# Performance work log

Measured on AMD Instinct MI355X. Metric: run time of the kernel, lower is better.

## Reference

```python
import jax, jax.numpy as jnp
import numpy as np

E = 8          # num experts
D = 1024       # hidden/model dim
H = 4096
B, S = 4, 2048


def setup_inputs() -> dict:
    key = jax.random.key(0)
    ks = jax.random.split(key, 4)
    x = jax.random.normal(ks[0], (B, S, D), dtype=jnp.float32)
    Wg = jax.random.normal(ks[1], (D, E), dtype=jnp.float32) * (1.0 / np.sqrt(D))
    W1 = jax.random.normal(ks[2], (E, D, H), dtype=jnp.float32) * (1.0 / np.sqrt(D))
    b1 = jnp.zeros((E, H), dtype=jnp.float32)
    W2 = jax.random.normal(ks[3], (E, H, D), dtype=jnp.float32) * (1.0 / np.sqrt(H))
    b2 = jnp.zeros((E, D), dtype=jnp.float32)
    return {"x": x, "Wg": Wg, "W1": W1, "b1": b1, "W2": W2, "b2": b2, "top_k": 2}


def reference(x, Wg, W1, b1, W2, b2, top_k):
    b, s, d = x.shape
    xt = x.reshape(-1, d)  # [T, D], T = total tokens
    # Linear gating: softmax over expert logits, select top_k, renormalize
    logits = xt @ Wg                                   # [T, E]
    probs = jax.nn.softmax(logits, axis=-1)            # [T, E]
    vals, idx = jax.lax.top_k(probs, top_k)            # [T, k]
    vals = vals / jnp.sum(vals, axis=-1, keepdims=True)
    # Combine weights: zero except at selected experts
    combine = jnp.sum(jax.nn.one_hot(idx, E, dtype=probs.dtype) * vals[..., None], axis=1)  # [T, E]
    # FFN experts (MLP with gelu), computed densely across experts
    h = jax.nn.gelu(jnp.einsum('td,edh->eth', xt, W1) + b1[:, None, :])  # [E, T, H]
    y = jnp.einsum('eth,ehd->etd', h, W2) + b2[:, None, :]               # [E, T, D]
    out = jnp.einsum('te,etd->td', combine, y)                           # [T, D]
    return out.reshape(b, s, d)
```

## Files before the change

### kernel.cpp

```cpp
#include <hip/hip_runtime.h>

#define T_TOK 8192
#define DIM   1024
#define HDIM  4096
#define NE    8
#define BK    64
#define BM    128
#define BN    128
#define SLOT_CAP (T_TOK * 2 + NE * BM)
#define TILES (SLOT_CAP / BM)

typedef float        f32x4 __attribute__((ext_vector_type(4)));
typedef unsigned int u32x4 __attribute__((ext_vector_type(4)));

__device__ inline unsigned short f2bf(float f) {
  union { float f; unsigned int u; } a; a.f = f;
  unsigned int u = a.u;
  unsigned int r = (u + 0x7FFFu + ((u >> 16) & 1u)) >> 16;
  return (unsigned short)r;
}

__device__ inline f32x4 mfma_bf16_16x16x32(u32x4 a, u32x4 b, f32x4 c) {
  asm("v_mfma_f32_16x16x32_bf16 %0, %1, %2, %0" : "+v"(c) : "v"(a), "v"(b));
  return c;
}

__device__ inline void gload_lds16(const void* g, void* l) {
  __builtin_amdgcn_global_load_lds(
      (const __attribute__((address_space(1))) void*)g,
      (__attribute__((address_space(3))) void*)l, 16, 0, 0);
}

__device__ inline float gelu_fast(float v) {
  const float c2 = 1.5957691216057308f;
  float z = c2 * (v + 0.044715f * v * v * v);
  return v / (1.0f + __expf(-z));
}

__global__ __launch_bounds__(256) void transpose_bf16_kernel(const float* __restrict__ src,
                                                             unsigned short* __restrict__ dst,
                                                             int R, int C) {
  __shared__ float tile[64][65];
  int e  = blockIdx.z;
  int c0 = blockIdx.x * 64, r0 = blockIdx.y * 64;
  int c  = threadIdx.x & 63, r4 = threadIdx.x >> 6;
  const float* s = src + (size_t)e * R * C;
#pragma unroll
  for (int i = 0; i < 16; i++) {
    int r = r4 + i * 4;
    tile[r][c] = s[(size_t)(r0 + r) * C + (c0 + c)];
  }
  __syncthreads();
  int cc = (threadIdx.x & 31) * 2;
  int rb = threadIdx.x >> 5;
  unsigned short* d = dst + (size_t)e * R * C;
#pragma unroll
  for (int i = 0; i < 8; i++) {
    int rr = rb + i * 8;
    unsigned int p = (unsigned int)f2bf(tile[cc][rr])
                   | ((unsigned int)f2bf(tile[cc + 1][rr]) << 16);
    *(unsigned int*)(d + (size_t)(c0 + rr) * R + (r0 + cc)) = p;
  }
}

__global__ __launch_bounds__(256) void routing_kernel(const float* __restrict__ x,
                                                      const float* __restrict__ Wg,
                                                      int* __restrict__ tok_e,
                                                      float* __restrict__ tok_w,
                                                      unsigned short* __restrict__ xb) {
  int tok  = (blockIdx.x * 256 + threadIdx.x) >> 6;
  int lane = threadIdx.x & 63;
  const float* xr = x + (size_t)tok * DIM;
  float acc[NE];
#pragma unroll
  for (int e = 0; e < NE; e++) acc[e] = 0.f;
  for (int d = lane; d < DIM; d += 64) {
    float xv = xr[d];
    const float* wr = Wg + d * NE;
#pragma unroll
    for (int e = 0; e < NE; e++) acc[e] += xv * wr[e];
  }
#pragma unroll
  for (int e = 0; e < NE; e++) {
#pragma unroll
    for (int off = 32; off > 0; off >>= 1) acc[e] += __shfl_xor(acc[e], off);
  }
  if (lane == 0) {
    int i0 = 0;
#pragma unroll
    for (int e = 1; e < NE; e++) if (acc[e] > acc[i0]) i0 = e;
    int i1 = (i0 == 0) ? 1 : 0;
#pragma unroll
    for (int e = 0; e < NE; e++) if (e != i0 && acc[e] > acc[i1]) i1 = e;
    float w0 = 1.0f / (1.0f + expf(acc[i1] - acc[i0]));
    tok_e[tok * 2]     = i0;
    tok_e[tok * 2 + 1] = i1;
    tok_w[tok * 2]     = w0;
    tok_w[tok * 2 + 1] = 1.0f - w0;
  }
  unsigned short* xo = xb + (size_t)tok * DIM;
#pragma unroll
  for (int i = 0; i < 4; i++) {
    f32x4 v = *(const f32x4*)(xr + lane * 16 + i * 4);
    unsigned long long p = (unsigned long long)f2bf(v[0])
                         | ((unsigned long long)f2bf(v[1]) << 16)
                         | ((unsigned long long)f2bf(v[2]) << 32)
                         | ((unsigned long long)f2bf(v[3]) << 48);
    *(unsigned long long*)(xo + lane * 16 + i * 4) = p;
  }
}

__global__ __launch_bounds__(256) void count_kernel(const int* __restrict__ tok_e,
                                                    int* __restrict__ counts) {
  __shared__ int h[NE];
  if (threadIdx.x < NE) h[threadIdx.x] = 0;
  __syncthreads();
  for (int i = blockIdx.x * 256 + threadIdx.x; i < T_TOK * 2; i += 32 * 256)
    atomicAdd(&h[tok_e[i]], 1);
  __syncthreads();
  if (threadIdx.x < NE) atomicAdd(&counts[threadIdx.x], h[threadIdx.x]);
}

__global__ void offsets_kernel(const int* __restrict__ counts, int* __restrict__ offs) {
  if (threadIdx.x == 0 && blockIdx.x == 0) {
    int acc = 0; offs[0] = 0;
    for (int e = 0; e < NE; e++) {
      acc += (counts[e] + BM - 1) / BM * BM;
      offs[e + 1] = acc;
    }
  }
}

__global__ __launch_bounds__(256) void scatter_kernel(const int* __restrict__ tok_e,
                                                      const int* __restrict__ offs,
                                                      int* __restrict__ cursors,
                                                      int* __restrict__ slot_token,
                                                      int* __restrict__ tok_slot) {
  int t = blockIdx.x * 256 + threadIdx.x;
  int lane = threadIdx.x & 63;
#pragma unroll
  for (int j = 0; j < 2; j++) {
    int e = tok_e[t * 2 + j];
#pragma unroll
    for (int ee = 0; ee < NE; ee++) {
      unsigned long long m = __ballot(e == ee);
      if (e == ee) {
        int leader = __ffsll(m) - 1;
        int base = 0;
        if (lane == leader) base = atomicAdd(&cursors[ee], (int)__popcll(m));
        base = __shfl(base, leader);
        int pos = base + (int)__popcll(m & ((1ULL << lane) - 1ULL));
        int s = offs[ee] + pos;
        slot_token[s] = t;
        tok_slot[t * 2 + j] = s;
      }
    }
  }
}


__global__ __launch_bounds__(256) void gemm1_kernel(const unsigned short* __restrict__ Xb,
                                                    const unsigned short* __restrict__ W1T,
                                                    const float* __restrict__ b1,
                                                    const int* __restrict__ slot_token,
                                                    const int* __restrict__ offs,
                                                    unsigned short* __restrict__ Hbuf) {
  __shared__ __align__(16) unsigned short As[BM][BK];
  __shared__ __align__(16) unsigned short Bs[BN][BK];
  const int GY = HDIM / BN;
  int lin = blockIdx.y * gridDim.x + blockIdx.x;
  int cpx = (TILES * GY) >> 3;
  int wk  = (lin & 7) * cpx + (lin >> 3);
  int bx = wk / GY, by = wk % GY;

  int row0 = bx * BM;
  if (row0 >= offs[NE]) return;
  int e = 0;
#pragma unroll
  for (int i = 1; i < NE; i++) if (row0 >= offs[i]) e = i;
  int n0  = by * BN;
  int tid  = threadIdx.x;
  int lane = tid & 63;
  int w    = tid >> 6;
  int wr = tid >> 7;
  int wc = (tid >> 6) & 1;

  int lr  = lane >> 3;
  int lcx = (lane & 7) ^ lr;
  const unsigned short* aG[4];
  const unsigned short* bG[4];
  unsigned short* aL[4];
  unsigned short* bL[4];
#pragma unroll
  for (int i = 0; i < 4; i++) {
    int r = w * 32 + i * 8;
    int tk = slot_token[row0 + r + lr];
    if (tk < 0) tk = 0;
    aG[i] = Xb + (size_t)tk * DIM + lcx * 8;
    bG[i] = W1T + ((size_t)e * HDIM + n0 + r + lr) * DIM + lcx * 8;
    aL[i] = &As[r][0];
    bL[i] = &Bs[r][0];
  }

  int frow = lane & 15;
  int hi   = lane >> 4;
  int kxs  = (hi * 8) ^ ((lane & 7) << 3);

  f32x4 acc[4][4];
#pragma unroll
  for (int m = 0; m < 4; m++)
#pragma unroll
    for (int n = 0; n < 4; n++) acc[m][n] = 0.f;

  for (int k0 = 0; k0 < DIM; k0 += BK) {
#pragma unroll
    for (int i = 0; i < 4; i++) gload_lds16(aG[i] + k0, aL[i]);
#pragma unroll
    for (int i = 0; i < 4; i++) gload_lds16(bG[i] + k0, bL[i]);
    __syncthreads();
#pragma unroll
    for (int kk = 0; kk < 2; kk++) {
      int col = (kk * 32) ^ kxs;
      u32x4 a[4], b[4];
#pragma unroll
      for (int m = 0; m < 4; m++)
        a[m] = *(const u32x4*)&As[wr * 64 + m * 16 + frow][col];
#pragma unroll
      for (int n = 0; n < 4; n++)
        b[n] = *(const u32x4*)&Bs[wc * 64 + n * 16 + frow][col];
#pragma unroll
      for (int m = 0; m < 4; m++)
#pragma unroll
        for (int n = 0; n < 4; n++)
          acc[m][n] = mfma_bf16_16x16x32(a[m], b[n], acc[m][n]);
    }
    __syncthreads();
  }

  float bias[4];
#pragma unroll
  for (int n = 0; n < 4; n++) bias[n] = b1[e * HDIM + n0 + wc * 64 + n * 16 + frow];
  unsigned short (*E)[136] = (unsigned short (*)[136])(&As[0][0]);
#pragma unroll
  for (int c0 = 0; c0 < 128; c0 += 32) {
    if (wr == (c0 >> 6)) {
      int mbase = (c0 & 63) >> 4;
#pragma unroll
      for (int mm = 0; mm < 2; mm++) {
        int m = mbase + mm;
#pragma unroll
        for (int n = 0; n < 4; n++)
#pragma unroll
          for (int j = 0; j < 4; j++)
            E[mm * 16 + hi * 4 + j][wc * 64 + n * 16 + frow] =
                f2bf(gelu_fast(acc[m][n][j] + bias[n]));
      }
    }
    __syncthreads();
#pragma unroll
    for (int p = 0; p < 2; p++) {
      int r  = p * 16 + (tid >> 4);
      int cc = (tid & 15) * 8;
      u32x4 v = *(const u32x4*)&E[r][cc];
      *(u32x4*)(Hbuf + (size_t)(row0 + c0 + r) * HDIM + n0 + cc) = v;
    }
    __syncthreads();
  }
}

__global__ __launch_bounds__(256) void gemm2_kernel(const unsigned short* __restrict__ Hbuf,
                                                    const unsigned short* __restrict__ W2T,
                                                    const float* __restrict__ b2,
                                                    const int* __restrict__ offs,
                                                    float* __restrict__ Ybuf) {
  __shared__ __align__(16) unsigned short As[BM][BK];
  __shared__ __align__(16) unsigned short Bs[BN][BK];
  const int GY = DIM / BN;
  int lin = blockIdx.y * gridDim.x + blockIdx.x;
  int cpx = (TILES * GY) >> 3;
  int wk  = (lin & 7) * cpx + (lin >> 3);
  int bx = wk / GY, by = wk % GY;

  int row0 = bx * BM;
  if (row0 >= offs[NE]) return;
  int e = 0;
#pragma unroll
  for (int i = 1; i < NE; i++) if (row0 >= offs[i]) e = i;
  int n0  = by * BN;
  int tid  = threadIdx.x;
  int lane = tid & 63;
  int w    = tid >> 6;
  int wr = tid >> 7;
  int wc = (tid >> 6) & 1;

  int lr  = lane >> 3;
  int lcx = (lane & 7) ^ lr;
  const unsigned short* aG[4];
  const unsigned short* bG[4];
  unsigned short* aL[4];
  unsigned short* bL[4];
#pragma unroll
  for (int i = 0; i < 4; i++) {
    int r = w * 32 + i * 8;
    aG[i] = Hbuf + (size_t)(row0 + r + lr) * HDIM + lcx * 8;
    bG[i] = W2T + ((size_t)e * DIM + n0 + r + lr) * HDIM + lcx * 8;
    aL[i] = &As[r][0];
    bL[i] = &Bs[r][0];
  }

  int frow = lane & 15;
  int kxs  = ((lane >> 4) * 8) ^ ((lane & 7) << 3);

  f32x4 acc[4][4];
#pragma unroll
  for (int m = 0; m < 4; m++)
#pragma unroll
    for (int n = 0; n < 4; n++) acc[m][n] = 0.f;

  for (int k0 = 0; k0 < HDIM; k0 += BK) {
#pragma unroll
    for (int i = 0; i < 4; i++) gload_lds16(aG[i] + k0, aL[i]);
#pragma unroll
    for (int i = 0; i < 4; i++) gload_lds16(bG[i] + k0, bL[i]);
    __syncthreads();
#pragma unroll
    for (int kk = 0; kk < 2; kk++) {
      int col = (kk * 32) ^ kxs;
      u32x4 a[4], b[4];
#pragma unroll
      for (int m = 0; m < 4; m++)
        a[m] = *(const u32x4*)&As[wr * 64 + m * 16 + frow][col];
#pragma unroll
      for (int n = 0; n < 4; n++)
        b[n] = *(const u32x4*)&Bs[wc * 64 + n * 16 + frow][col];
#pragma unroll
      for (int m = 0; m < 4; m++)
#pragma unroll
        for (int n = 0; n < 4; n++)
          acc[m][n] = mfma_bf16_16x16x32(a[m], b[n], acc[m][n]);
    }
    __syncthreads();
  }

  int rbase = (lane >> 4) * 4;
  int cbase = lane & 15;
#pragma unroll
  for (int m = 0; m < 4; m++) {
#pragma unroll
    for (int n = 0; n < 4; n++) {
      int dcol = n0 + wc * 64 + n * 16 + cbase;
      float bias = b2[e * DIM + dcol];
#pragma unroll
      for (int j = 0; j < 4; j++) {
        int gr = row0 + wr * 64 + m * 16 + rbase + j;
        Ybuf[(size_t)gr * DIM + dcol] = acc[m][n][j] + bias;
      }
    }
  }
}

__global__ __launch_bounds__(256) void combine_kernel(const float* __restrict__ Ybuf,
                                                      const int* __restrict__ tok_slot,
                                                      const float* __restrict__ tok_w,
                                                      float* __restrict__ out) {
  int t = blockIdx.x;
  int c = threadIdx.x * 4;
  int s0 = tok_slot[t * 2], s1 = tok_slot[t * 2 + 1];
  float w0 = tok_w[t * 2], w1 = tok_w[t * 2 + 1];
  f32x4 y0 = *(const f32x4*)(Ybuf + (size_t)s0 * DIM + c);
  f32x4 y1 = *(const f32x4*)(Ybuf + (size_t)s1 * DIM + c);
  f32x4 r;
#pragma unroll
  for (int i = 0; i < 4; i++) r[i] = w0 * y0[i] + w1 * y1[i];
  *(f32x4*)(out + (size_t)t * DIM + c) = r;
}

extern "C" void kernel_launch(void* const* d_in, const int* in_sizes, int n_in,
                              void* d_out, int out_size, void* d_ws, size_t ws_size,
                              hipStream_t stream) {
  (void)in_sizes; (void)n_in; (void)out_size;
  const float* x  = (const float*)d_in[0];
  const float* Wg = (const float*)d_in[1];
  const float* W1 = (const float*)d_in[2];
  const float* b1 = (const float*)d_in[3];
  const float* W2 = (const float*)d_in[4];
  const float* b2 = (const float*)d_in[5];
  float* out = (float*)d_out;

  char* ws = (char*)d_ws;
  size_t off = 0;
  auto take = [&](size_t bytes) -> char* {
    char* p = ws + off;
    off += (bytes + 255) & ~(size_t)255;
    return p;
  };
  unsigned short* W1T  = (unsigned short*)take((size_t)NE * DIM * HDIM * 2);
  unsigned short* W2T  = (unsigned short*)take((size_t)NE * DIM * HDIM * 2);
  unsigned short* Xb   = (unsigned short*)take((size_t)T_TOK * DIM * 2);
  unsigned short* Hbuf = (unsigned short*)take((size_t)SLOT_CAP * HDIM * 2);
  float* Ybuf       = (float*)take((size_t)SLOT_CAP * DIM * 4);
  int*   slot_token = (int*)take(SLOT_CAP * 4);
  int*   tok_e      = (int*)take(T_TOK * 2 * 4);
  float* tok_w      = (float*)take(T_TOK * 2 * 4);
  int*   tok_slot   = (int*)take(T_TOK * 2 * 4);
  int*   counts     = (int*)take(256);
  int*   cursors    = (int*)take(256);
  int*   offs       = (int*)take(256);

  if (off > ws_size) {
    hipMemsetAsync(d_out, 0, (size_t)out_size * 4, stream);
    return;
  }

  hipMemsetAsync(counts, 0, 256, stream);
  hipMemsetAsync(cursors, 0, 256, stream);
  hipMemsetAsync(slot_token, 0xFF, SLOT_CAP * 4, stream);

  routing_kernel<<<T_TOK / 4, 256, 0, stream>>>(x, Wg, tok_e, tok_w, Xb);
  count_kernel<<<32, 256, 0, stream>>>(tok_e, counts);
  offsets_kernel<<<1, 64, 0, stream>>>(counts, offs);
  scatter_kernel<<<T_TOK / 256, 256, 0, stream>>>(tok_e, offs, cursors, slot_token, tok_slot);
  transpose_bf16_kernel<<<dim3(HDIM / 64, DIM / 64, NE), 256, 0, stream>>>(W1, W1T, DIM, HDIM);
  transpose_bf16_kernel<<<dim3(DIM / 64, HDIM / 64, NE), 256, 0, stream>>>(W2, W2T, HDIM, DIM);
  gemm1_kernel<<<dim3(TILES, HDIM / BN), 256, 0, stream>>>(Xb, W1T, b1, slot_token, offs, Hbuf);
  gemm2_kernel<<<dim3(TILES, DIM / BN), 256, 0, stream>>>(Hbuf, W2T, b2, offs, Ybuf);
  combine_kernel<<<T_TOK, 256, 0, stream>>>(Ybuf, tok_slot, tok_w, out);
}
```

Baseline: 534.8 us.

## Fuse expert counting into routing, store Y in bf16, vectorize transpose writes

Expert histogram counting moves into the routing kernel, and the offsets kernel is removed by having each consumer compute offsets from the counts. The gemm2 output is staged through LDS and stored as bf16 with 16-byte writes, which halves Ybuf traffic, and the combine kernel reads that bf16. The transpose kernel writes 16-byte vectors instead of 4-byte ones. Together these cut two kernel launches and memory traffic, at the cost of extra rounding of expert outputs to bf16 before the weighted combine.

```diff
diff --git a/kernel.cpp b/kernel.cpp
--- a/kernel.cpp
+++ b/kernel.cpp
@@ -37,6 +37,13 @@
   return v / (1.0f + __expf(-z));
 }
 
+__device__ inline void load_offs(const int* __restrict__ counts, int* offs) {
+  offs[0] = 0;
+#pragma unroll
+  for (int e = 0; e < NE; e++)
+    offs[e + 1] = offs[e] + ((counts[e] + BM - 1) / BM) * BM;
+}
+
 __global__ __launch_bounds__(256) void transpose_bf16_kernel(const float* __restrict__ src,
                                                              unsigned short* __restrict__ dst,
                                                              int R, int C) {
@@ -51,15 +58,17 @@
     tile[r][c] = s[(size_t)(r0 + r) * C + (c0 + c)];
   }
   __syncthreads();
-  int cc = (threadIdx.x & 31) * 2;
-  int rb = threadIdx.x >> 5;
   unsigned short* d = dst + (size_t)e * R * C;
-#pragma unroll
-  for (int i = 0; i < 8; i++) {
-    int rr = rb + i * 8;
-    unsigned int p = (unsigned int)f2bf(tile[cc][rr])
-                   | ((unsigned int)f2bf(tile[cc + 1][rr]) << 16);
-    *(unsigned int*)(d + (size_t)(c0 + rr) * R + (r0 + cc)) = p;
+  int rbase = (threadIdx.x & 7) * 8;
+#pragma unroll
+  for (int g = 0; g < 2; g++) {
+    int cc = (threadIdx.x >> 3) + g * 32;
+    u32x4 v;
+#pragma unroll
+    for (int k = 0; k < 4; k++)
+      v[k] = (unsigned int)f2bf(tile[rbase + 2 * k][cc])
+           | ((unsigned int)f2bf(tile[rbase + 2 * k + 1][cc]) << 16);
+    *(u32x4*)(d + (size_t)(c0 + cc) * R + (r0 + rbase)) = v;
   }
 }
 
@@ -67,7 +76,11 @@
                                                       const float* __restrict__ Wg,
                                                       int* __restrict__ tok_e,
                                                       float* __restrict__ tok_w,
-                                                      unsigned short* __restrict__ xb) {
+                                                      unsigned short* __restrict__ xb,
+                                                      int* __restrict__ counts) {
+  __shared__ int h[NE];
+  if (threadIdx.x < NE) h[threadIdx.x] = 0;
+  __syncthreads();
   int tok  = (blockIdx.x * 256 + threadIdx.x) >> 6;
   int lane = threadIdx.x & 63;
   const float* xr = x + (size_t)tok * DIM;
@@ -97,6 +110,8 @@
     tok_e[tok * 2 + 1] = i1;
     tok_w[tok * 2]     = w0;
     tok_w[tok * 2 + 1] = 1.0f - w0;
+    atomicAdd(&h[i0], 1);
+    atomicAdd(&h[i1], 1);
   }
   unsigned short* xo = xb + (size_t)tok * DIM;
 #pragma unroll
@@ -108,34 +123,17 @@
                          | ((unsigned long long)f2bf(v[3]) << 48);
     *(unsigned long long*)(xo + lane * 16 + i * 4) = p;
   }
-}
-
-__global__ __launch_bounds__(256) void count_kernel(const int* __restrict__ tok_e,
-                                                    int* __restrict__ counts) {
-  __shared__ int h[NE];
-  if (threadIdx.x < NE) h[threadIdx.x] = 0;
-  __syncthreads();
-  for (int i = blockIdx.x * 256 + threadIdx.x; i < T_TOK * 2; i += 32 * 256)
-    atomicAdd(&h[tok_e[i]], 1);
   __syncthreads();
   if (threadIdx.x < NE) atomicAdd(&counts[threadIdx.x], h[threadIdx.x]);
 }
 
-__global__ void offsets_kernel(const int* __restrict__ counts, int* __restrict__ offs) {
-  if (threadIdx.x == 0 && blockIdx.x == 0) {
-    int acc = 0; offs[0] = 0;
-    for (int e = 0; e < NE; e++) {
-      acc += (counts[e] + BM - 1) / BM * BM;
-      offs[e + 1] = acc;
-    }
-  }
-}
-
 __global__ __launch_bounds__(256) void scatter_kernel(const int* __restrict__ tok_e,
-                                                      const int* __restrict__ offs,
+                                                      const int* __restrict__ counts,
                                                       int* __restrict__ cursors,
                                                       int* __restrict__ slot_token,
                                                       int* __restrict__ tok_slot) {
+  int offs[NE + 1];
+  load_offs(counts, offs);
   int t = blockIdx.x * 256 + threadIdx.x;
   int lane = threadIdx.x & 63;
 #pragma unroll
@@ -163,10 +161,12 @@
                                                     const unsigned short* __restrict__ W1T,
                                                     const float* __restrict__ b1,
                                                     const int* __restrict__ slot_token,
-                                                    const int* __restrict__ offs,
+                                                    const int* __restrict__ counts,
                                                     unsigned short* __restrict__ Hbuf) {
   __shared__ __align__(16) unsigned short As[BM][BK];
   __shared__ __align__(16) unsigned short Bs[BN][BK];
+  int offs[NE + 1];
+  load_offs(counts, offs);
   const int GY = HDIM / BN;
   int lin = blockIdx.y * gridDim.x + blockIdx.x;
   int cpx = (TILES * GY) >> 3;
@@ -271,10 +271,12 @@
 __global__ __launch_bounds__(256) void gemm2_kernel(const unsigned short* __restrict__ Hbuf,
                                                     const unsigned short* __restrict__ W2T,
                                                     const float* __restrict__ b2,
-                                                    const int* __restrict__ offs,
-                                                    float* __restrict__ Ybuf) {
+                                                    const int* __restrict__ counts,
+                                                    unsigned short* __restrict__ Ybuf) {
   __shared__ __align__(16) unsigned short As[BM][BK];
   __shared__ __align__(16) unsigned short Bs[BN][BK];
+  int offs[NE + 1];
+  load_offs(counts, offs);
   const int GY = DIM / BN;
   int lin = blockIdx.y * gridDim.x + blockIdx.x;
   int cpx = (TILES * GY) >> 3;
@@ -309,7 +311,8 @@
   }
 
   int frow = lane & 15;
-  int kxs  = ((lane >> 4) * 8) ^ ((lane & 7) << 3);
+  int hi   = lane >> 4;
+  int kxs  = (hi * 8) ^ ((lane & 7) << 3);
 
   f32x4 acc[4][4];
 #pragma unroll
@@ -342,37 +345,59 @@
     __syncthreads();
   }
 
-  int rbase = (lane >> 4) * 4;
-  int cbase = lane & 15;
-#pragma unroll
-  for (int m = 0; m < 4; m++) {
-#pragma unroll
-    for (int n = 0; n < 4; n++) {
-      int dcol = n0 + wc * 64 + n * 16 + cbase;
-      float bias = b2[e * DIM + dcol];
-#pragma unroll
-      for (int j = 0; j < 4; j++) {
-        int gr = row0 + wr * 64 + m * 16 + rbase + j;
-        Ybuf[(size_t)gr * DIM + dcol] = acc[m][n][j] + bias;
+  float bias[4];
+#pragma unroll
+  for (int n = 0; n < 4; n++) bias[n] = b2[e * DIM + n0 + wc * 64 + n * 16 + frow];
+  unsigned short (*E)[136] = (unsigned short (*)[136])(&As[0][0]);
+#pragma unroll
+  for (int c0 = 0; c0 < 128; c0 += 32) {
+    if (wr == (c0 >> 6)) {
+      int mbase = (c0 & 63) >> 4;
+#pragma unroll
+      for (int mm = 0; mm < 2; mm++) {
+        int m = mbase + mm;
+#pragma unroll
+        for (int n = 0; n < 4; n++)
+#pragma unroll
+          for (int j = 0; j < 4; j++)
+            E[mm * 16 + hi * 4 + j][wc * 64 + n * 16 + frow] =
+                f2bf(acc[m][n][j] + bias[n]);
       }
     }
-  }
-}
-
-__global__ __launch_bounds__(256) void combine_kernel(const float* __restrict__ Ybuf,
+    __syncthreads();
+#pragma unroll
+    for (int p = 0; p < 2; p++) {
+      int r  = p * 16 + (tid >> 4);
+      int cc = (tid & 15) * 8;
+      u32x4 v = *(const u32x4*)&E[r][cc];
+      *(u32x4*)(Ybuf + (size_t)(row0 + c0 + r) * DIM + n0 + cc) = v;
+    }
+    __syncthreads();
+  }
+}
+
+__global__ __launch_bounds__(256) void combine_kernel(const unsigned short* __restrict__ Ybuf,
                                                       const int* __restrict__ tok_slot,
                                                       const float* __restrict__ tok_w,
                                                       float* __restrict__ out) {
-  int t = blockIdx.x;
-  int c = threadIdx.x * 4;
+  int t = blockIdx.x * 2 + (threadIdx.x >> 7);
+  int c = (threadIdx.x & 127) * 8;
   int s0 = tok_slot[t * 2], s1 = tok_slot[t * 2 + 1];
   float w0 = tok_w[t * 2], w1 = tok_w[t * 2 + 1];
-  f32x4 y0 = *(const f32x4*)(Ybuf + (size_t)s0 * DIM + c);
-  f32x4 y1 = *(const f32x4*)(Ybuf + (size_t)s1 * DIM + c);
-  f32x4 r;
-#pragma unroll
-  for (int i = 0; i < 4; i++) r[i] = w0 * y0[i] + w1 * y1[i];
-  *(f32x4*)(out + (size_t)t * DIM + c) = r;
+  u32x4 y0 = *(const u32x4*)(Ybuf + (size_t)s0 * DIM + c);
+  u32x4 y1 = *(const u32x4*)(Ybuf + (size_t)s1 * DIM + c);
+  float r[8];
+#pragma unroll
+  for (int k = 0; k < 4; k++) {
+    union { unsigned int u; float f; } a0, b0, a1, b1;
+    a0.u = y0[k] << 16; b0.u = y0[k] & 0xFFFF0000u;
+    a1.u = y1[k] << 16; b1.u = y1[k] & 0xFFFF0000u;
+    r[2 * k]     = w0 * a0.f + w1 * a1.f;
+    r[2 * k + 1] = w0 * b0.f + w1 * b1.f;
+  }
+  float* o = out + (size_t)t * DIM + c;
+  *(f32x4*)o       = *(f32x4*)&r[0];
+  *(f32x4*)(o + 4) = *(f32x4*)&r[4];
 }
 
 extern "C" void kernel_launch(void* const* d_in, const int* in_sizes, int n_in,
@@ -398,14 +423,13 @@
   unsigned short* W2T  = (unsigned short*)take((size_t)NE * DIM * HDIM * 2);
   unsigned short* Xb   = (unsigned short*)take((size_t)T_TOK * DIM * 2);
   unsigned short* Hbuf = (unsigned short*)take((size_t)SLOT_CAP * HDIM * 2);
-  float* Ybuf       = (float*)take((size_t)SLOT_CAP * DIM * 4);
+  unsigned short* Ybuf = (unsigned short*)take((size_t)SLOT_CAP * DIM * 2);
   int*   slot_token = (int*)take(SLOT_CAP * 4);
   int*   tok_e      = (int*)take(T_TOK * 2 * 4);
   float* tok_w      = (float*)take(T_TOK * 2 * 4);
   int*   tok_slot   = (int*)take(T_TOK * 2 * 4);
   int*   counts     = (int*)take(256);
   int*   cursors    = (int*)take(256);
-  int*   offs       = (int*)take(256);
 
   if (off > ws_size) {
     hipMemsetAsync(d_out, 0, (size_t)out_size * 4, stream);
@@ -416,13 +440,11 @@
   hipMemsetAsync(cursors, 0, 256, stream);
   hipMemsetAsync(slot_token, 0xFF, SLOT_CAP * 4, stream);
 
-  routing_kernel<<<T_TOK / 4, 256, 0, stream>>>(x, Wg, tok_e, tok_w, Xb);
-  count_kernel<<<32, 256, 0, stream>>>(tok_e, counts);
-  offsets_kernel<<<1, 64, 0, stream>>>(counts, offs);
-  scatter_kernel<<<T_TOK / 256, 256, 0, stream>>>(tok_e, offs, cursors, slot_token, tok_slot);
+  routing_kernel<<<T_TOK / 4, 256, 0, stream>>>(x, Wg, tok_e, tok_w, Xb, counts);
+  scatter_kernel<<<T_TOK / 256, 256, 0, stream>>>(tok_e, counts, cursors, slot_token, tok_slot);
   transpose_bf16_kernel<<<dim3(HDIM / 64, DIM / 64, NE), 256, 0, stream>>>(W1, W1T, DIM, HDIM);
   transpose_bf16_kernel<<<dim3(DIM / 64, HDIM / 64, NE), 256, 0, stream>>>(W2, W2T, HDIM, DIM);
-  gemm1_kernel<<<dim3(TILES, HDIM / BN), 256, 0, stream>>>(Xb, W1T, b1, slot_token, offs, Hbuf);
-  gemm2_kernel<<<dim3(TILES, DIM / BN), 256, 0, stream>>>(Hbuf, W2T, b2, offs, Ybuf);
-  combine_kernel<<<T_TOK, 256, 0, stream>>>(Ybuf, tok_slot, tok_w, out);
-}
+  gemm1_kernel<<<dim3(TILES, HDIM / BN), 256, 0, stream>>>(Xb, W1T, b1, slot_token, counts, Hbuf);
+  gemm2_kernel<<<dim3(TILES, DIM / BN), 256, 0, stream>>>(Hbuf, W2T, b2, counts, Ybuf);
+  combine_kernel<<<T_TOK / 2, 256, 0, stream>>>(Ybuf, tok_slot, tok_w, out);
+}
```

Result: no change. 531.3 us (-0.6%).
